# Performance work log

Measured on AMD Instinct MI355X. Metric: run time of the kernel, lower is better.

The kernel has to match this reference:

```python
import jax, jax.numpy as jnp
import numpy as np
import math

B, S, D, H = 2, 2048, 1024, 16
DK = D // H


def setup_inputs() -> dict:
    key = jax.random.key(0)
    ks = jax.random.split(key, 12)
    std = 1.0 / math.sqrt(D)
    inp = {
        "query": jax.random.normal(ks[0], (B, S, D), jnp.float32),
        "key_": jax.random.normal(ks[1], (B, S, D), jnp.float32),
        "value": jax.random.normal(ks[2], (B, S, D), jnp.float32),
        # causal mask: True = masked out
        "attn_mask": jnp.triu(jnp.ones((S, S), jnp.bool_), k=1),
        "w_q": jax.random.uniform(ks[3], (D, D), jnp.float32, -std, std),
        "b_q": jax.random.uniform(ks[4], (D,), jnp.float32, -std, std),
        "w_k": jax.random.uniform(ks[5], (D, D), jnp.float32, -std, std),
        "b_k": jax.random.uniform(ks[6], (D,), jnp.float32, -std, std),
        "w_v": jax.random.uniform(ks[7], (D, D), jnp.float32, -std, std),
        "b_v": jax.random.uniform(ks[8], (D,), jnp.float32, -std, std),
        "w_o": jax.random.uniform(ks[9], (D, D), jnp.float32, -std, std),
        "b_o": jax.random.uniform(ks[10], (D,), jnp.float32, -std, std),
    }
    return inp


def reference(query, key_, value, attn_mask, w_q, b_q, w_k, b_k, w_v, b_v, w_o, b_o):
    # linear projections (torch Linear: x @ W.T + b)
    q = query @ w_q.T + b_q
    k = key_ @ w_k.T + b_k
    v = value @ w_v.T + b_v
    # [B, H, S, DK]
    q = q.reshape(B, S, H, DK).transpose(0, 2, 1, 3)
    k = k.reshape(B, S, H, DK).transpose(0, 2, 1, 3)
    v = v.reshape(B, S, H, DK).transpose(0, 2, 1, 3)
    scores = jnp.einsum("bhqd,bhkd->bhqk", q, k) / jnp.sqrt(jnp.float32(DK))
    scores = jnp.where(attn_mask[None, None, :, :], -jnp.inf, scores)
    attn = jax.nn.softmax(scores, axis=-1)
    context = jnp.einsum("bhqk,bhkd->bhqd", attn, v)
    context = context.transpose(0, 2, 1, 3).reshape(B, S, D)
    return context @ w_o.T + b_o
```

## Files before the change

### kernel.cpp

```cpp
#include <hip/hip_runtime.h>

#define B_ 2
#define S_ 2048
#define D_ 1024
#define H_ 16
#define DK_ 64
#define K_ 1024

typedef __bf16 bf16x8 __attribute__((ext_vector_type(8)));
typedef __bf16 bf16x4 __attribute__((ext_vector_type(4)));
typedef float f32x4 __attribute__((ext_vector_type(4)));

#define QSCALE 0.18033688011112042f

__device__ __forceinline__ void gload16(const void* g, void* l) {
    __builtin_amdgcn_global_load_lds(
        (const __attribute__((address_space(1))) unsigned int*)g,
        (__attribute__((address_space(3))) unsigned int*)l, 16, 0, 0);
}

__device__ __forceinline__ bf16x8 cvt8f(const float* __restrict__ p) {
    f32x4 a = *reinterpret_cast<const f32x4*>(p);
    f32x4 b = *reinterpret_cast<const f32x4*>(p + 4);
    bf16x8 r;
#pragma unroll
    for (int j = 0; j < 4; ++j) { r[j] = (__bf16)a[j]; r[j + 4] = (__bf16)b[j]; }
    return r;
}

__global__ __launch_bounds__(256) void cvt3(
    const float* __restrict__ s0, const float* __restrict__ s1, const float* __restrict__ s2,
    __bf16* __restrict__ d0, __bf16* __restrict__ d1, __bf16* __restrict__ d2, int n8)
{
    const float* s; __bf16* d;
    if (blockIdx.y == 0) { s = s0; d = d0; }
    else if (blockIdx.y == 1) { s = s1; d = d1; }
    else { s = s2; d = d2; }
    int i = blockIdx.x * 256 + threadIdx.x;
    if (i >= n8) return;
    *reinterpret_cast<bf16x8*>(d + (size_t)i * 8) = cvt8f(s + (size_t)i * 8);
}

__global__ __launch_bounds__(256) void cvt4(
    const float* __restrict__ s0, const float* __restrict__ s1,
    const float* __restrict__ s2, const float* __restrict__ s3,
    __bf16* __restrict__ d0, __bf16* __restrict__ d1,
    __bf16* __restrict__ d2, __bf16* __restrict__ d3, int n8)
{
    const float* s; __bf16* d;
    if (blockIdx.y == 0) { s = s0; d = d0; }
    else if (blockIdx.y == 1) { s = s1; d = d1; }
    else if (blockIdx.y == 2) { s = s2; d = d2; }
    else { s = s3; d = d3; }
    int i = blockIdx.x * 256 + threadIdx.x;
    if (i >= n8) return;
    *reinterpret_cast<bf16x8*>(d + (size_t)i * 8) = cvt8f(s + (size_t)i * 8);
}

__global__ __launch_bounds__(512) void gemm_qkv256(
    const __bf16* __restrict__ qin, const __bf16* __restrict__ kin, const __bf16* __restrict__ vin,
    const __bf16* __restrict__ wq,  const __bf16* __restrict__ wk,  const __bf16* __restrict__ wv,
    const float* __restrict__ bq,   const float* __restrict__ bk,   const float* __restrict__ bv,
    __bf16* __restrict__ qo, __bf16* __restrict__ ko, __bf16* __restrict__ vto)
{
    __shared__ __attribute__((aligned(16))) char lds[4][32768];

    const int tid = threadIdx.x;
    const int w = tid >> 6, lane = tid & 63;
    const int l15 = lane & 15, lh = lane >> 4;
    const int wr = w >> 2, wc = w & 3;

    const int z = blockIdx.y;
    const __bf16* A; const __bf16* Bm; const float* bias;
    int brow, bcol;
    if (z == 0)      { A = qin; Bm = wq;  bias = bq; brow = (blockIdx.x & 15) * 256; bcol = (blockIdx.x >> 4) * 256; }
    else if (z == 1) { A = kin; Bm = wk;  bias = bk; brow = (blockIdx.x & 15) * 256; bcol = (blockIdx.x >> 4) * 256; }
    else             { A = wv;  Bm = vin; bias = bv; brow = (blockIdx.x & 3)  * 256; bcol = (blockIdx.x >> 2) * 256; }

    const char* Ab = (const char*)A;
    const char* Bb = (const char*)Bm;

    auto stageAB = [&](int tt, int p) {
        char* base = lds[tt & 3];
        const char* src = (p == 0) ? Ab : Bb;
        const int rowbase = (p == 0) ? brow : bcol;
        const int dsto = (p == 0) ? 0 : 16384;
        const int koff = tt * 64;
#pragma unroll
        for (int j = 0; j < 2; ++j) {
            const int s    = j * 512 + tid;
            const int row  = s >> 2;
            const int slot = s & 3;
            const int scol = (slot ^ ((row >> 1) & 3)) * 16;
            const int loff = __builtin_amdgcn_readfirstlane(dsto + (j * 512 + w * 64) * 16);
            gload16(src + (size_t)(rowbase + row) * 2048 + koff + scol, base + loff);
        }
    };

    auto readA = [&](int buf, int msub) -> bf16x8 {
        const int hrow = wr * 128 + msub * 16 + l15;
        const int off  = hrow * 64 + ((lh << 4) ^ ((hrow & 6) << 3));
        return *reinterpret_cast<const bf16x8*>(&lds[buf][off]);
    };
    auto readB = [&](int buf, int nsub) -> bf16x8 {
        const int hrow = wc * 64 + nsub * 16 + l15;
        const int off  = 16384 + hrow * 64 + ((lh << 4) ^ ((hrow & 6) << 3));
        return *reinterpret_cast<const bf16x8*>(&lds[buf][off]);
    };

    f32x4 acc[8][4] = {};
    const int NT = K_ / 32;

    stageAB(0, 0); stageAB(0, 1); stageAB(1, 0); stageAB(1, 1);
    asm volatile("s_waitcnt vmcnt(4)" ::: "memory");
    __builtin_amdgcn_s_barrier();

    bf16x8 bfr[4];
    for (int t = 0; t < NT; ++t) {
        const int buf = t & 3;
#pragma unroll
        for (int p = 0; p < 2; ++p) {
            bf16x8 af[4];
#pragma unroll
            for (int i = 0; i < 4; ++i) af[i] = readA(buf, p * 4 + i);
            if (p == 0) {
#pragma unroll
                for (int n = 0; n < 4; ++n) bfr[n] = readB(buf, n);
            }
            if (t + 2 < NT) stageAB(t + 2, p);
            if (p == 1) {
                if (t < NT - 2)       { asm volatile("s_waitcnt vmcnt(4)" ::: "memory"); }
                else if (t == NT - 2) { asm volatile("s_waitcnt vmcnt(0)" ::: "memory"); }
            }
            __builtin_amdgcn_s_barrier();
            asm volatile("s_waitcnt lgkmcnt(0)" ::: "memory");
            __builtin_amdgcn_sched_barrier(0);
            __builtin_amdgcn_s_setprio(1);
#pragma unroll
            for (int i = 0; i < 4; ++i)
#pragma unroll
                for (int n = 0; n < 4; ++n)
                    acc[p * 4 + i][n] = __builtin_amdgcn_mfma_f32_16x16x32_bf16(
                        af[i], bfr[n], acc[p * 4 + i][n], 0, 0, 0);
            __builtin_amdgcn_s_setprio(0);
        }
    }

#pragma unroll
    for (int ni = 0; ni < 4; ++ni) {
        const int n = bcol + wc * 64 + ni * 16 + l15;
#pragma unroll
        for (int mi = 0; mi < 8; ++mi)
#pragma unroll
            for (int r = 0; r < 4; ++r) {
                const int m = brow + wr * 128 + mi * 16 + lh * 4 + r;
                if (z < 2) {
                    float v = acc[mi][ni][r] + bias[n];
                    if (z == 0) v *= QSCALE;
                    const int bb = m >> 11, ss = m & (S_ - 1);
                    const int hh = n >> 6,  dk = n & 63;
                    __bf16* o = (z == 0) ? qo : ko;
                    o[(((size_t)(bb * H_ + hh)) * S_ + ss) * DK_ + dk] = (__bf16)v;
                } else {
                    const float v = acc[mi][ni][r] + bias[m];
                    const int hh = m >> 6,  dk = m & 63;
                    const int bb = n >> 11, ss = n & (S_ - 1);
                    vto[(((size_t)(bb * H_ + hh)) * DK_ + dk) * S_ + ss] = (__bf16)v;
                }
            }
    }
}

__device__ __forceinline__ void gemm_body_dbuf(
    const char* __restrict__ Ab, const char* __restrict__ Bb,
    int brow, int bcol, __bf16* ldsA, __bf16* ldsB, f32x4 (&acc)[4][4])
{
    const int tid = threadIdx.x;
    const int w = tid >> 6, lane = tid & 63;
    const int l15 = lane & 15, lh = lane >> 4;
    const int wr = w >> 1, wc = w & 1;
    const int srow  = lane >> 2;
    const int scolb = (lane & 3) * 16;

    auto stage = [&](int buf, int k0) {
#pragma unroll
        for (int c = 0; c < 2; ++c) {
            const int chunk = w * 2 + c;
            const int row   = chunk * 16 + srow;
            const int loff  = __builtin_amdgcn_readfirstlane(buf * 8192 + chunk * 1024);
            gload16(Ab + (size_t)(brow + row) * 2048 + k0 * 2 + scolb, (char*)ldsA + loff);
            gload16(Bb + (size_t)(bcol + row) * 2048 + k0 * 2 + scolb, (char*)ldsB + loff);
        }
    };

    stage(0, 0);
    int buf = 0;
    for (int k0 = 0; k0 < K_; k0 += 32) {
        if (k0 + 32 < K_) {
            stage(buf ^ 1, k0 + 32);
            asm volatile("s_waitcnt vmcnt(4)" ::: "memory");
        } else {
            asm volatile("s_waitcnt vmcnt(0)" ::: "memory");
        }
        __builtin_amdgcn_s_barrier();
        __builtin_amdgcn_sched_barrier(0);

        const int bo = buf * 4096;
        bf16x8 af[4], bfr[4];
#pragma unroll
        for (int m = 0; m < 4; ++m)
            af[m] = *reinterpret_cast<const bf16x8*>(&ldsA[bo + (wr * 64 + m * 16 + l15) * 32 + lh * 8]);
#pragma unroll
        for (int n = 0; n < 4; ++n)
            bfr[n] = *reinterpret_cast<const bf16x8*>(&ldsB[bo + (wc * 64 + n * 16 + l15) * 32 + lh * 8]);

        __builtin_amdgcn_s_setprio(1);
#pragma unroll
        for (int m = 0; m < 4; ++m)
#pragma unroll
            for (int n = 0; n < 4; ++n)
                acc[m][n] = __builtin_amdgcn_mfma_f32_16x16x32_bf16(af[m], bfr[n], acc[m][n], 0, 0, 0);
        __builtin_amdgcn_s_setprio(0);

        __builtin_amdgcn_s_barrier();
        buf ^= 1;
    }
}

__global__ __launch_bounds__(256) void gemm_out(
    const __bf16* __restrict__ A, const __bf16* __restrict__ Bm,
    const float* __restrict__ bias, float* __restrict__ out)
{
    __shared__ __attribute__((aligned(16))) __bf16 ldsA[2 * 128 * 32];
    __shared__ __attribute__((aligned(16))) __bf16 ldsB[2 * 128 * 32];

    const int brow = blockIdx.x * 128;
    const int bcol = blockIdx.y * 128;

    f32x4 acc[4][4] = {};
    gemm_body_dbuf((const char*)A, (const char*)Bm, brow, bcol, ldsA, ldsB, acc);

    const int tid = threadIdx.x;
    const int w = tid >> 6, lane = tid & 63;
    const int l15 = lane & 15, lh = lane >> 4;
    const int wr = w >> 1, wc = w & 1;

#pragma unroll
    for (int ni = 0; ni < 4; ++ni) {
        const int n = bcol + wc * 64 + ni * 16 + l15;
        const float bv = bias[n];
#pragma unroll
        for (int mi = 0; mi < 4; ++mi)
#pragma unroll
            for (int r = 0; r < 4; ++r) {
                const int m = brow + wr * 64 + mi * 16 + lh * 4 + r;
                out[(size_t)m * D_ + n] = acc[mi][ni][r] + bv;
            }
    }
}

__global__ __launch_bounds__(256, 4) void attn_kernel(
    const __bf16* __restrict__ Q, const __bf16* __restrict__ K,
    const __bf16* __restrict__ VT, __bf16* __restrict__ CTX)
{
    __shared__ __attribute__((aligned(16))) char ldsK[2][8192];
    __shared__ __attribute__((aligned(16))) char ldsV[2][8192];
    __shared__ __attribute__((aligned(16))) __bf16 p_lds[4][16][64];

    const int tid = threadIdx.x;
    const int w = tid >> 6, l = tid & 63;
    const int l15 = l & 15, lh = l >> 4;

    const int panel = 31 - (int)(blockIdx.x >> 5);
    const int bhidx = blockIdx.x & 31;
    const int h = bhidx & 15;
    const int b = bhidx >> 4;

    const size_t bh = (size_t)(b * H_ + h);
    const __bf16* qp   = Q + bh * S_ * DK_;
    const char*  kbase = (const char*)(K  + bh * S_ * DK_);
    const char*  vbase = (const char*)(VT + bh * DK_ * S_);

    const int np = panel + 1;
    const int wave_base = panel * 64 + w * 16;

    const int srow = l >> 3;
    const int ssw  = ((l & 7) * 16) ^ (srow * 16);

    auto stage = [&](int pos) {
        const int k0 = pos * 64;
        char* lk = ldsK[pos & 1];
        char* lv = ldsV[pos & 1];
#pragma unroll
        for (int i = 0; i < 2; ++i) {
            const int r0   = w * 16 + i * 8;
            const int loff = __builtin_amdgcn_readfirstlane(r0 * 128);
            gload16(kbase + (size_t)(k0 + r0 + srow) * 128 + ssw, lk + loff);
            gload16(vbase + (size_t)(r0 + srow) * 4096 + (size_t)k0 * 2 + ssw, lv + loff);
        }
    };

    bf16x8 aq[2];
#pragma unroll
    for (int c = 0; c < 2; ++c)
        aq[c] = *reinterpret_cast<const bf16x8*>(
            qp + (size_t)(wave_base + l15) * DK_ + c * 32 + lh * 8);

    bf16x8 vones;
#pragma unroll
    for (int j = 0; j < 8; ++j) vones[j] = (__bf16)1.0f;
    const f32x4 fzero = {0.f, 0.f, 0.f, 0.f};

    f32x4 acc[4] = {};
    f32x4 acc_l = {};
    float mrun = -INFINITY;

    stage(0);

    for (int it = 0; it < np; ++it) {
        if (it + 1 < np) {
            stage(it + 1);
            asm volatile("s_waitcnt vmcnt(4)" ::: "memory");
        } else {
            asm volatile("s_waitcnt vmcnt(0)" ::: "memory");
        }
        __builtin_amdgcn_s_barrier();
        __builtin_amdgcn_sched_barrier(0);

        const int k0 = it * 64;
        const char* lk = ldsK[it & 1];
        const char* lv = ldsV[it & 1];

        bf16x8 ak[4][2];
#pragma unroll
        for (int t = 0; t < 4; ++t)
#pragma unroll
            for (int c = 0; c < 2; ++c) {
                const int col = (c * 64 + lh * 16) ^ ((l15 & 7) << 4);
                ak[t][c] = *reinterpret_cast<const bf16x8*>(lk + (t * 16 + l15) * 128 + col);
            }

        f32x4 sacc[4];
        __builtin_amdgcn_s_setprio(1);
#pragma unroll
        for (int t = 0; t < 4; ++t) {
            sacc[t] = __builtin_amdgcn_mfma_f32_16x16x32_bf16(ak[t][0], aq[0], fzero, 0, 0, 0);
            sacc[t] = __builtin_amdgcn_mfma_f32_16x16x32_bf16(ak[t][1], aq[1], sacc[t], 0, 0, 0);
        }
        __builtin_amdgcn_s_setprio(0);

        bf16x8 bv[4][2];
#pragma unroll
        for (int nt = 0; nt < 4; ++nt)
#pragma unroll
            for (int c2 = 0; c2 < 2; ++c2) {
                const int col = (c2 * 64 + lh * 16) ^ ((l15 & 7) << 4);
                bv[nt][c2] = *reinterpret_cast<const bf16x8*>(lv + (nt * 16 + l15) * 128 + col);
            }

        if (k0 + 63 > wave_base) {
            const int qa = wave_base + l15;
#pragma unroll
            for (int t = 0; t < 4; ++t)
#pragma unroll
                for (int r = 0; r < 4; ++r) {
                    const int ka = k0 + t * 16 + lh * 4 + r;
                    if (ka > qa) sacc[t][r] = -INFINITY;
                }
        }

        f32x4 m4 = sacc[0];
#pragma unroll
        for (int t = 1; t < 4; ++t)
#pragma unroll
            for (int r = 0; r < 4; ++r) m4[r] = fmaxf(m4[r], sacc[t][r]);
        float rm = fmaxf(fmaxf(m4[0], m4[1]), fmaxf(m4[2], m4[3]));
        rm = fmaxf(rm, __shfl_xor(rm, 16, 64));
        rm = fmaxf(rm, __shfl_xor(rm, 32, 64));

        if (!__all(rm <= mrun + 8.f)) {
            const float mnew = fmaxf(mrun, rm);
            const float scl  = exp2f(mrun - mnew);
            mrun = mnew;
#pragma unroll
            for (int r = 0; r < 4; ++r) {
                const float sr = __shfl(scl, lh * 4 + r, 64);
#pragma unroll
                for (int nt = 0; nt < 4; ++nt) acc[nt][r] *= sr;
                acc_l[r] *= sr;
            }
        }

#pragma unroll
        for (int t = 0; t < 4; ++t) {
            bf16x4 pk;
#pragma unroll
            for (int r = 0; r < 4; ++r)
                pk[r] = (__bf16)exp2f(sacc[t][r] - mrun);
            const int wcol = (t * 16 + lh * 4) ^ ((l15 & 7) << 3);
            *reinterpret_cast<bf16x4*>(&p_lds[w][l15][wcol]) = pk;
        }

        bf16x8 pa[2];
#pragma unroll
        for (int c2 = 0; c2 < 2; ++c2) {
            const int rcol = (c2 * 32 + lh * 8) ^ ((l15 & 7) << 3);
            pa[c2] = *reinterpret_cast<const bf16x8*>(&p_lds[w][l15][rcol]);
        }

        __builtin_amdgcn_s_setprio(1);
#pragma unroll
        for (int nt = 0; nt < 4; ++nt)
#pragma unroll
            for (int c2 = 0; c2 < 2; ++c2)
                acc[nt] = __builtin_amdgcn_mfma_f32_16x16x32_bf16(
                    pa[c2], bv[nt][c2], acc[nt], 0, 0, 0);
        acc_l = __builtin_amdgcn_mfma_f32_16x16x32_bf16(pa[0], vones, acc_l, 0, 0, 0);
        acc_l = __builtin_amdgcn_mfma_f32_16x16x32_bf16(pa[1], vones, acc_l, 0, 0, 0);
        __builtin_amdgcn_s_setprio(0);

        __builtin_amdgcn_s_barrier();
    }

#pragma unroll
    for (int r = 0; r < 4; ++r) {
        const float linv = 1.f / acc_l[r];
        const int srow2 = wave_base + lh * 4 + r;
#pragma unroll
        for (int nt = 0; nt < 4; ++nt)
            CTX[((size_t)b * S_ + srow2) * D_ + h * DK_ + nt * 16 + l15] =
                (__bf16)(acc[nt][r] * linv);
    }
}

extern "C" void kernel_launch(void* const* d_in, const int* in_sizes, int n_in,
                              void* d_out, int out_size, void* d_ws, size_t ws_size,
                              hipStream_t stream) {
    (void)in_sizes; (void)n_in; (void)out_size; (void)ws_size;

    const float* query = (const float*)d_in[0];
    const float* key_  = (const float*)d_in[1];
    const float* value = (const float*)d_in[2];
    const float* w_q = (const float*)d_in[4];
    const float* b_q = (const float*)d_in[5];
    const float* w_k = (const float*)d_in[6];
    const float* b_k = (const float*)d_in[7];
    const float* w_v = (const float*)d_in[8];
    const float* b_v = (const float*)d_in[9];
    const float* w_o = (const float*)d_in[10];
    const float* b_o = (const float*)d_in[11];
    float* out = (float*)d_out;

    char* Wp = (char*)d_ws;
    const size_t MB = 1024 * 1024;
    __bf16* qin = (__bf16*)(Wp + 0 * MB);
    __bf16* kin = (__bf16*)(Wp + 8 * MB);
    __bf16* vin = (__bf16*)(Wp + 16 * MB);
    __bf16* wq  = (__bf16*)(Wp + 24 * MB);
    __bf16* wk  = (__bf16*)(Wp + 26 * MB);
    __bf16* wv  = (__bf16*)(Wp + 28 * MB);
    __bf16* wo  = (__bf16*)(Wp + 30 * MB);
    __bf16* q   = (__bf16*)(Wp + 32 * MB);
    __bf16* k   = (__bf16*)(Wp + 40 * MB);
    __bf16* vt  = (__bf16*)(Wp + 48 * MB);
    __bf16* ctx = qin;

    const int n8_big = (B_ * S_ * D_) / 8;
    const int n8_w   = (D_ * D_) / 8;

    hipLaunchKernelGGL(cvt3, dim3(n8_big / 256, 3), dim3(256), 0, stream,
                       query, key_, value, qin, kin, vin, n8_big);
    hipLaunchKernelGGL(cvt4, dim3(n8_w / 256, 4), dim3(256), 0, stream,
                       w_q, w_k, w_v, w_o, wq, wk, wv, wo, n8_w);
    hipLaunchKernelGGL(gemm_qkv256, dim3(64, 3), dim3(512), 0, stream,
                       qin, kin, vin, wq, wk, wv, b_q, b_k, b_v, q, k, vt);
    hipLaunchKernelGGL(attn_kernel, dim3(1024), dim3(256), 0, stream,
                       q, k, vt, ctx);
    hipLaunchKernelGGL(gemm_out, dim3(32, 8), dim3(256), 0, stream,
                       ctx, wo, b_o, out);
}
```

Measured before the change: 134.6 us.

## Fuse fp32-to-bf16 activation conversion into QKV GEMM and rebalance attention panels

Removes the separate cvt3 pass that converted query/key/value to bf16 in workspace. The QKV projection GEMM now reads fp32 activations directly through registers, converts them, and writes them into LDS, which saves a full read/write round trip of three 16MB-equivalent tensors. The GEMM tile shrinks from 256x256 with 512 threads to 128x128 with 256 threads and double buffering, so the grid has more blocks but less reuse per block. The attention kernel also reorders panel assignment so that long and short causal panels interleave, to balance load across CUs.

```diff
diff --git a/kernel.cpp b/kernel.cpp
--- a/kernel.cpp
+++ b/kernel.cpp
@@ -26,19 +26,6 @@
 #pragma unroll
     for (int j = 0; j < 4; ++j) { r[j] = (__bf16)a[j]; r[j + 4] = (__bf16)b[j]; }
     return r;
-}
-
-__global__ __launch_bounds__(256) void cvt3(
-    const float* __restrict__ s0, const float* __restrict__ s1, const float* __restrict__ s2,
-    __bf16* __restrict__ d0, __bf16* __restrict__ d1, __bf16* __restrict__ d2, int n8)
-{
-    const float* s; __bf16* d;
-    if (blockIdx.y == 0) { s = s0; d = d0; }
-    else if (blockIdx.y == 1) { s = s1; d = d1; }
-    else { s = s2; d = d2; }
-    int i = blockIdx.x * 256 + threadIdx.x;
-    if (i >= n8) return;
-    *reinterpret_cast<bf16x8*>(d + (size_t)i * 8) = cvt8f(s + (size_t)i * 8);
 }
 
 __global__ __launch_bounds__(256) void cvt4(
@@ -57,92 +44,100 @@
     *reinterpret_cast<bf16x8*>(d + (size_t)i * 8) = cvt8f(s + (size_t)i * 8);
 }
 
-__global__ __launch_bounds__(512) void gemm_qkv256(
-    const __bf16* __restrict__ qin, const __bf16* __restrict__ kin, const __bf16* __restrict__ vin,
+__global__ __launch_bounds__(256) void gemm_qkv(
+    const float* __restrict__ query, const float* __restrict__ key_, const float* __restrict__ value,
     const __bf16* __restrict__ wq,  const __bf16* __restrict__ wk,  const __bf16* __restrict__ wv,
     const float* __restrict__ bq,   const float* __restrict__ bk,   const float* __restrict__ bv,
     __bf16* __restrict__ qo, __bf16* __restrict__ ko, __bf16* __restrict__ vto)
 {
-    __shared__ __attribute__((aligned(16))) char lds[4][32768];
+    __shared__ __attribute__((aligned(16))) char ldsF[2][8192];
+    __shared__ __attribute__((aligned(16))) char ldsL[2][8192];
 
     const int tid = threadIdx.x;
     const int w = tid >> 6, lane = tid & 63;
     const int l15 = lane & 15, lh = lane >> 4;
-    const int wr = w >> 2, wc = w & 3;
-
-    const int z = blockIdx.y;
-    const __bf16* A; const __bf16* Bm; const float* bias;
+    const int wr = w >> 1, wc = w & 1;
+
+    const int z = blockIdx.z;
     int brow, bcol;
-    if (z == 0)      { A = qin; Bm = wq;  bias = bq; brow = (blockIdx.x & 15) * 256; bcol = (blockIdx.x >> 4) * 256; }
-    else if (z == 1) { A = kin; Bm = wk;  bias = bk; brow = (blockIdx.x & 15) * 256; bcol = (blockIdx.x >> 4) * 256; }
-    else             { A = wv;  Bm = vin; bias = bv; brow = (blockIdx.x & 3)  * 256; bcol = (blockIdx.x >> 2) * 256; }
-
-    const char* Ab = (const char*)A;
-    const char* Bb = (const char*)Bm;
-
-    auto stageAB = [&](int tt, int p) {
-        char* base = lds[tt & 3];
-        const char* src = (p == 0) ? Ab : Bb;
-        const int rowbase = (p == 0) ? brow : bcol;
-        const int dsto = (p == 0) ? 0 : 16384;
-        const int koff = tt * 64;
-#pragma unroll
-        for (int j = 0; j < 2; ++j) {
-            const int s    = j * 512 + tid;
-            const int row  = s >> 2;
-            const int slot = s & 3;
-            const int scol = (slot ^ ((row >> 1) & 3)) * 16;
-            const int loff = __builtin_amdgcn_readfirstlane(dsto + (j * 512 + w * 64) * 16);
-            gload16(src + (size_t)(rowbase + row) * 2048 + koff + scol, base + loff);
-        }
+    if (z < 2) { brow = blockIdx.x * 128; bcol = blockIdx.y * 128; }
+    else       { brow = (blockIdx.x & 7) * 128; bcol = (blockIdx.y * 4 + (blockIdx.x >> 3)) * 128; }
+
+    const float* Fsrc = (z == 0) ? query : (z == 1) ? key_ : value;
+    const int    Frow = (z < 2) ? brow : bcol;
+    const char*  Lsrc = (const char*)((z == 0) ? wq : (z == 1) ? wk : wv);
+    const int    Lrow = (z < 2) ? bcol : brow;
+
+    const int fr = tid >> 1, fch = tid & 1;
+    const float* fbase = Fsrc + (size_t)(Frow + fr) * 1024 + fch * 16;
+
+    const int srow = lane >> 2, scolb = (lane & 3) * 16;
+
+    f32x4 areg[4];
+    auto loadF = [&](int k0) {
+#pragma unroll
+        for (int j = 0; j < 4; ++j)
+            areg[j] = *reinterpret_cast<const f32x4*>(fbase + k0 + j * 4);
     };
-
-    auto readA = [&](int buf, int msub) -> bf16x8 {
-        const int hrow = wr * 128 + msub * 16 + l15;
-        const int off  = hrow * 64 + ((lh << 4) ^ ((hrow & 6) << 3));
-        return *reinterpret_cast<const bf16x8*>(&lds[buf][off]);
+    auto writeF = [&](int buf) {
+        bf16x8 lo, hi;
+#pragma unroll
+        for (int j = 0; j < 4; ++j) { lo[j] = (__bf16)areg[0][j]; lo[j+4] = (__bf16)areg[1][j];
+                                      hi[j] = (__bf16)areg[2][j]; hi[j+4] = (__bf16)areg[3][j]; }
+        char* dst = &ldsF[buf][fr * 64 + fch * 32];
+        *reinterpret_cast<bf16x8*>(dst) = lo;
+        *reinterpret_cast<bf16x8*>(dst + 16) = hi;
     };
-    auto readB = [&](int buf, int nsub) -> bf16x8 {
-        const int hrow = wc * 64 + nsub * 16 + l15;
-        const int off  = 16384 + hrow * 64 + ((lh << 4) ^ ((hrow & 6) << 3));
-        return *reinterpret_cast<const bf16x8*>(&lds[buf][off]);
+    auto stageL = [&](int buf, int k0) {
+#pragma unroll
+        for (int c = 0; c < 2; ++c) {
+            const int chunk = w * 2 + c;
+            const int loff  = __builtin_amdgcn_readfirstlane(chunk * 1024);
+            gload16(Lsrc + (size_t)(Lrow + chunk * 16 + srow) * 2048 + k0 * 2 + scolb,
+                    &ldsL[buf][loff]);
+        }
     };
 
-    f32x4 acc[8][4] = {};
+    const char* aLds = (z < 2) ? &ldsF[0][0] : &ldsL[0][0];
+    const char* bLds = (z < 2) ? &ldsL[0][0] : &ldsF[0][0];
+
+    f32x4 acc[4][4] = {};
     const int NT = K_ / 32;
 
-    stageAB(0, 0); stageAB(0, 1); stageAB(1, 0); stageAB(1, 1);
-    asm volatile("s_waitcnt vmcnt(4)" ::: "memory");
+    loadF(0); stageL(0, 0);
+    asm volatile("s_waitcnt vmcnt(0)" ::: "memory");
+    writeF(0);
+    loadF(32); stageL(1, 32);
+    asm volatile("s_waitcnt lgkmcnt(0)" ::: "memory");
     __builtin_amdgcn_s_barrier();
 
-    bf16x8 bfr[4];
     for (int t = 0; t < NT; ++t) {
-        const int buf = t & 3;
-#pragma unroll
-        for (int p = 0; p < 2; ++p) {
-            bf16x8 af[4];
-#pragma unroll
-            for (int i = 0; i < 4; ++i) af[i] = readA(buf, p * 4 + i);
-            if (p == 0) {
-#pragma unroll
-                for (int n = 0; n < 4; ++n) bfr[n] = readB(buf, n);
-            }
-            if (t + 2 < NT) stageAB(t + 2, p);
-            if (p == 1) {
-                if (t < NT - 2)       { asm volatile("s_waitcnt vmcnt(4)" ::: "memory"); }
-                else if (t == NT - 2) { asm volatile("s_waitcnt vmcnt(0)" ::: "memory"); }
-            }
+        const int buf = t & 1;
+        const int bo  = buf * 8192;
+
+        bf16x8 af[4], bfr[4];
+#pragma unroll
+        for (int m = 0; m < 4; ++m)
+            af[m] = *reinterpret_cast<const bf16x8*>(aLds + bo + (wr * 64 + m * 16 + l15) * 64 + lh * 16);
+#pragma unroll
+        for (int n = 0; n < 4; ++n)
+            bfr[n] = *reinterpret_cast<const bf16x8*>(bLds + bo + (wc * 64 + n * 16 + l15) * 64 + lh * 16);
+
+        __builtin_amdgcn_s_setprio(1);
+#pragma unroll
+        for (int m = 0; m < 4; ++m)
+#pragma unroll
+            for (int n = 0; n < 4; ++n)
+                acc[m][n] = __builtin_amdgcn_mfma_f32_16x16x32_bf16(af[m], bfr[n], acc[m][n], 0, 0, 0);
+        __builtin_amdgcn_s_setprio(0);
+
+        if (t + 1 < NT) {
+            asm volatile("s_waitcnt vmcnt(0)" ::: "memory");
             __builtin_amdgcn_s_barrier();
+            writeF(buf ^ 1);
+            if (t + 2 < NT) { loadF((t + 2) * 32); stageL(buf, (t + 2) * 32); }
             asm volatile("s_waitcnt lgkmcnt(0)" ::: "memory");
-            __builtin_amdgcn_sched_barrier(0);
-            __builtin_amdgcn_s_setprio(1);
-#pragma unroll
-            for (int i = 0; i < 4; ++i)
-#pragma unroll
-                for (int n = 0; n < 4; ++n)
-                    acc[p * 4 + i][n] = __builtin_amdgcn_mfma_f32_16x16x32_bf16(
-                        af[i], bfr[n], acc[p * 4 + i][n], 0, 0, 0);
-            __builtin_amdgcn_s_setprio(0);
+            __builtin_amdgcn_s_barrier();
         }
     }
 
@@ -150,19 +145,19 @@
     for (int ni = 0; ni < 4; ++ni) {
         const int n = bcol + wc * 64 + ni * 16 + l15;
 #pragma unroll
-        for (int mi = 0; mi < 8; ++mi)
+        for (int mi = 0; mi < 4; ++mi)
 #pragma unroll
             for (int r = 0; r < 4; ++r) {
-                const int m = brow + wr * 128 + mi * 16 + lh * 4 + r;
+                const int m = brow + wr * 64 + mi * 16 + lh * 4 + r;
                 if (z < 2) {
-                    float v = acc[mi][ni][r] + bias[n];
+                    float v = acc[mi][ni][r] + ((z == 0) ? bq[n] : bk[n]);
                     if (z == 0) v *= QSCALE;
                     const int bb = m >> 11, ss = m & (S_ - 1);
                     const int hh = n >> 6,  dk = n & 63;
                     __bf16* o = (z == 0) ? qo : ko;
                     o[(((size_t)(bb * H_ + hh)) * S_ + ss) * DK_ + dk] = (__bf16)v;
                 } else {
-                    const float v = acc[mi][ni][r] + bias[m];
+                    const float v = acc[mi][ni][r] + bv[m];
                     const int hh = m >> 6,  dk = m & 63;
                     const int bb = n >> 11, ss = n & (S_ - 1);
                     vto[(((size_t)(bb * H_ + hh)) * DK_ + dk) * S_ + ss] = (__bf16)v;
@@ -171,16 +166,23 @@
     }
 }
 
-__device__ __forceinline__ void gemm_body_dbuf(
-    const char* __restrict__ Ab, const char* __restrict__ Bb,
-    int brow, int bcol, __bf16* ldsA, __bf16* ldsB, f32x4 (&acc)[4][4])
+__global__ __launch_bounds__(256) void gemm_out(
+    const __bf16* __restrict__ A, const __bf16* __restrict__ Bm,
+    const float* __restrict__ bias, float* __restrict__ out)
 {
+    __shared__ __attribute__((aligned(16))) __bf16 ldsA[2 * 128 * 32];
+    __shared__ __attribute__((aligned(16))) __bf16 ldsB[2 * 128 * 32];
+
     const int tid = threadIdx.x;
     const int w = tid >> 6, lane = tid & 63;
     const int l15 = lane & 15, lh = lane >> 4;
     const int wr = w >> 1, wc = w & 1;
+    const int brow = blockIdx.x * 128;
+    const int bcol = blockIdx.y * 128;
     const int srow  = lane >> 2;
     const int scolb = (lane & 3) * 16;
+    const char* Ab = (const char*)A;
+    const char* Bb = (const char*)Bm;
 
     auto stage = [&](int buf, int k0) {
 #pragma unroll
@@ -193,6 +195,7 @@
         }
     };
 
+    f32x4 acc[4][4] = {};
     stage(0, 0);
     int buf = 0;
     for (int k0 = 0; k0 < K_; k0 += 32) {
@@ -225,25 +228,6 @@
         __builtin_amdgcn_s_barrier();
         buf ^= 1;
     }
-}
-
-__global__ __launch_bounds__(256) void gemm_out(
-    const __bf16* __restrict__ A, const __bf16* __restrict__ Bm,
-    const float* __restrict__ bias, float* __restrict__ out)
-{
-    __shared__ __attribute__((aligned(16))) __bf16 ldsA[2 * 128 * 32];
-    __shared__ __attribute__((aligned(16))) __bf16 ldsB[2 * 128 * 32];
-
-    const int brow = blockIdx.x * 128;
-    const int bcol = blockIdx.y * 128;
-
-    f32x4 acc[4][4] = {};
-    gemm_body_dbuf((const char*)A, (const char*)Bm, brow, bcol, ldsA, ldsB, acc);
-
-    const int tid = threadIdx.x;
-    const int w = tid >> 6, lane = tid & 63;
-    const int l15 = lane & 15, lh = lane >> 4;
-    const int wr = w >> 1, wc = w & 1;
 
 #pragma unroll
     for (int ni = 0; ni < 4; ++ni) {
@@ -271,8 +255,15 @@
     const int w = tid >> 6, l = tid & 63;
     const int l15 = l & 15, lh = l >> 4;
 
-    const int panel = 31 - (int)(blockIdx.x >> 5);
-    const int bhidx = blockIdx.x & 31;
+    const int c  = blockIdx.x & 255;
+    const int rr = blockIdx.x >> 8;
+    const int qq = c >> 5;
+    const int bhidx = c & 31;
+    int panel;
+    if (rr == 0)      panel = 31 - qq;
+    else if (rr == 1) panel = qq;
+    else if (rr == 2) panel = 23 - qq;
+    else              panel = 8 + qq;
     const int h = bhidx & 15;
     const int b = bhidx >> 4;
 
@@ -302,9 +293,9 @@
 
     bf16x8 aq[2];
 #pragma unroll
-    for (int c = 0; c < 2; ++c)
-        aq[c] = *reinterpret_cast<const bf16x8*>(
-            qp + (size_t)(wave_base + l15) * DK_ + c * 32 + lh * 8);
+    for (int cc = 0; cc < 2; ++cc)
+        aq[cc] = *reinterpret_cast<const bf16x8*>(
+            qp + (size_t)(wave_base + l15) * DK_ + cc * 32 + lh * 8);
 
     bf16x8 vones;
 #pragma unroll
@@ -335,9 +326,9 @@
 #pragma unroll
         for (int t = 0; t < 4; ++t)
 #pragma unroll
-            for (int c = 0; c < 2; ++c) {
-                const int col = (c * 64 + lh * 16) ^ ((l15 & 7) << 4);
-                ak[t][c] = *reinterpret_cast<const bf16x8*>(lk + (t * 16 + l15) * 128 + col);
+            for (int cc = 0; cc < 2; ++cc) {
+                const int col = (cc * 64 + lh * 16) ^ ((l15 & 7) << 4);
+                ak[t][cc] = *reinterpret_cast<const bf16x8*>(lk + (t * 16 + l15) * 128 + col);
             }
 
         f32x4 sacc[4];
@@ -453,9 +444,7 @@
 
     char* Wp = (char*)d_ws;
     const size_t MB = 1024 * 1024;
-    __bf16* qin = (__bf16*)(Wp + 0 * MB);
-    __bf16* kin = (__bf16*)(Wp + 8 * MB);
-    __bf16* vin = (__bf16*)(Wp + 16 * MB);
+    __bf16* ctx = (__bf16*)(Wp + 0 * MB);
     __bf16* wq  = (__bf16*)(Wp + 24 * MB);
     __bf16* wk  = (__bf16*)(Wp + 26 * MB);
     __bf16* wv  = (__bf16*)(Wp + 28 * MB);
@@ -463,17 +452,13 @@
     __bf16* q   = (__bf16*)(Wp + 32 * MB);
     __bf16* k   = (__bf16*)(Wp + 40 * MB);
     __bf16* vt  = (__bf16*)(Wp + 48 * MB);
-    __bf16* ctx = qin;
-
-    const int n8_big = (B_ * S_ * D_) / 8;
-    const int n8_w   = (D_ * D_) / 8;
-
-    hipLaunchKernelGGL(cvt3, dim3(n8_big / 256, 3), dim3(256), 0, stream,
-                       query, key_, value, qin, kin, vin, n8_big);
+
+    const int n8_w = (D_ * D_) / 8;
+
     hipLaunchKernelGGL(cvt4, dim3(n8_w / 256, 4), dim3(256), 0, stream,
                        w_q, w_k, w_v, w_o, wq, wk, wv, wo, n8_w);
-    hipLaunchKernelGGL(gemm_qkv256, dim3(64, 3), dim3(512), 0, stream,
-                       qin, kin, vin, wq, wk, wv, b_q, b_k, b_v, q, k, vt);
+    hipLaunchKernelGGL(gemm_qkv, dim3(32, 8, 3), dim3(256), 0, stream,
+                       query, key_, value, wq, wk, wv, b_q, b_k, b_v, q, k, vt);
     hipLaunchKernelGGL(attn_kernel, dim3(1024), dim3(256), 0, stream,
                        q, k, vt, ctx);
     hipLaunchKernelGGL(gemm_out, dim3(32, 8), dim3(256), 0, stream,
```

Measured after the change: 134.7 us. No clear change (+0.1%).
